# Optimization experiments

Hardware: AMD Instinct MI355X
Metric: run time of the kernel (lower is better)

The kernel has to match this reference:

```python
import jax, jax.numpy as jnp
import numpy as np

NB_CLASSES = 10  # matches init_kwargs nb_classes


def setup_inputs() -> dict:
    key = jax.random.key(0)
    k1, k2 = jax.random.split(key)
    N, D = 500_000, 64
    h = jax.random.normal(k1, (N, D), dtype=jnp.float32)
    yhat = jax.random.randint(k2, (N,), 0, NB_CLASSES, dtype=jnp.int32)
    return {"h": h, "yhat": yhat}


def reference(h, yhat):
    # Original torch loop: for each class k, gather h_k = h[yhat==k],
    # M_k = mean_i(h_i h_i^T) * 0.5 + I, loss += 0.5 * logdet(M_k).
    # mean of outer products == (masked h)^T @ h / count_k, so we avoid
    # the ragged gather and any [N, D, D] intermediate entirely.
    N, D = h.shape
    eye = jnp.eye(D, dtype=h.dtype)

    def class_term(k):
        mask = (yhat == k).astype(h.dtype)            # [N]
        count = jnp.sum(mask)                         # B_k
        gram = jnp.einsum('nd,ne->de', mask[:, None] * h, h)  # sum_i h_i h_i^T
        M = gram * (0.5 / count) + eye                # [D, D], SPD
        _, logabsdet = jnp.linalg.slogdet(M)
        return 0.5 * logabsdet

    # NB_CLASSES is a small fixed constant -> Python loop is fine & keeps
    # peak memory at one extra [N, D] buffer.
    return jnp.sum(jnp.stack([class_term(k) for k in range(NB_CLASSES)]))
```

## Files before the change

### kernel.cpp

```cpp
#include <hip/hip_runtime.h>
#include <hip/hip_bf16.h>

typedef __attribute__((ext_vector_type(8))) short    short8;
typedef __attribute__((ext_vector_type(4))) float    f32x4;
typedef __attribute__((ext_vector_type(4))) _Float16 f16x4;
typedef __attribute__((ext_vector_type(2))) unsigned u32x2;

#define NCLS 10
#define TILE 64
#define TPB  512
#define NQ   10
#define PPB  (NCLS * NQ * 256)
#define CH   16

#define AS1 __attribute__((address_space(1)))
#define AS3 __attribute__((address_space(3)))

#define MF(a, b, c) __builtin_amdgcn_mfma_f32_16x16x32_bf16((a), (b), (c), 0, 0, 0)

static __device__ __forceinline__ unsigned pkh2(float a, float b) {
    unsigned short ha = __builtin_bit_cast(unsigned short, (_Float16)a);
    unsigned short hb = __builtin_bit_cast(unsigned short, (_Float16)b);
    return (unsigned)ha | ((unsigned)hb << 16);
}

static __device__ __forceinline__ void issue_tile(
        const float* __restrict__ h, const int* __restrict__ yhat,
        float* fsb, int* yb, long t, long N, int wid, int lane) {
#pragma unroll
    for (int i = 0; i < 2; ++i) {
        const int C = (wid * 2 + i) * 64 + lane;
        long row = t * TILE + (C >> 4);
        if (row > N - 1) row = N - 1;
        const float* gp = h + row * 64 + ((C & 15) << 2);
        __builtin_amdgcn_global_load_lds((const AS1 float*)gp,
                                         (AS3 float*)(fsb + (wid * 2 + i) * 256),
                                         16, 0, 0);
    }
    if (wid == 0 && lane < 16) {
        long y0 = t * TILE + lane * 4;
        if (y0 > N - 4) y0 = N - 4;
        __builtin_amdgcn_global_load_lds((const AS1 int*)(yhat + y0),
                                         (AS3 int*)yb, 16, 0, 0);
    }
}

static __device__ __forceinline__ void compute_tile(
        const char* hsb, const char* mkb, int cls, int xcls, int wq,
        int hi, int col, f32x4 (&acc)[NQ], f32x4 (&accx)[3]) {
    const int sw = (col & 7) << 4;
#pragma unroll
    for (int ks = 0; ks < 2; ++ks) {
        const int b2 = ks * 64 + hi * 16;
        const short8 m = *(const short8*)(mkb + cls * 128 + b2);
        short8 raw[4], am[4];
#pragma unroll
        for (int nb = 0; nb < 4; ++nb) {
            raw[nb] = *(const short8*)(hsb + (nb * 16 + col) * 128 + (b2 ^ sw));
            am[nb]  = raw[nb] & m;
        }
        acc[0] = MF(am[0], am[0], acc[0]);
        acc[1] = MF(am[0], am[1], acc[1]);
        acc[2] = MF(am[0], am[2], acc[2]);
        acc[3] = MF(am[0], am[3], acc[3]);
        acc[4] = MF(am[1], am[1], acc[4]);
        acc[5] = MF(am[1], am[2], acc[5]);
        acc[6] = MF(am[1], am[3], acc[6]);
        acc[7] = MF(am[2], am[2], acc[7]);
        acc[8] = MF(am[2], am[3], acc[8]);
        acc[9] = MF(am[3], am[3], acc[9]);

        const short8 mx = *(const short8*)(mkb + xcls * 128 + b2);
        switch (wq) {
        case 0: { short8 x0 = raw[0] & mx, x1 = raw[1] & mx;
                  accx[0] = MF(x0, x0, accx[0]);
                  accx[1] = MF(x0, x1, accx[1]);
                  accx[2] = MF(x1, x1, accx[2]); } break;
        case 1: { short8 x0 = raw[0] & mx, x2 = raw[2] & mx, x3 = raw[3] & mx;
                  accx[0] = MF(x0, x2, accx[0]);
                  accx[1] = MF(x0, x3, accx[1]); } break;
        case 2: { short8 x1 = raw[1] & mx, x2 = raw[2] & mx, x3 = raw[3] & mx;
                  accx[0] = MF(x1, x2, accx[0]);
                  accx[1] = MF(x1, x3, accx[1]);
                  accx[2] = MF(x2, x2, accx[2]); } break;
        default:{ short8 x2 = raw[2] & mx, x3 = raw[3] & mx;
                  accx[0] = MF(x2, x3, accx[0]);
                  accx[1] = MF(x3, x3, accx[1]); } break;
        }
    }
}

__global__ __launch_bounds__(TPB, 4) void HL_gram(
        const float* __restrict__ h, const int* __restrict__ yhat,
        _Float16* __restrict__ partials, int* __restrict__ cntp,
        long N, int ntiles, int G) {
    __shared__ __align__(16) float          fs[3][TILE * 64];
    __shared__ __align__(16) unsigned short hs[2][64 * TILE];
    __shared__ __align__(16) unsigned short mk[2][NCLS * TILE];
    __shared__ __align__(16) int            ylds[3][TILE];

    const int tid  = threadIdx.x;
    const int wid  = tid >> 6;
    const int lane = tid & 63;
    const int hi   = lane >> 4;
    const int col  = lane & 15;

    const int cls  = wid;
    const int xcls = 8 + (wid >> 2);
    const int wq   = wid & 3;

    f32x4 acc[NQ], accx[3];
#pragma unroll
    for (int q = 0; q < NQ; ++q) acc[q] = (f32x4){0.f, 0.f, 0.f, 0.f};
#pragma unroll
    for (int q = 0; q < 3; ++q)  accx[q] = (f32x4){0.f, 0.f, 0.f, 0.f};
    int c0=0,c1=0,c2=0,c3=0,c4=0,c5=0,c6=0,c7=0,c8=0,c9=0;

    const int bid = blockIdx.x;
    const int K   = (ntiles - bid + G - 1) / G;

    issue_tile(h, yhat, &fs[0][0], &ylds[0][0], bid, N, wid, lane);
    if (K > 1)
        issue_tile(h, yhat, &fs[1][0], &ylds[1][0], bid + (long)G, N, wid, lane);

    for (int k = 0; k < K; ++k) {
        const long t  = bid + (long)k * G;
        const int  fk = k % 3;
        const int  hk = k & 1;

        if (k + 1 < K) {
            if (wid == 0) asm volatile("s_waitcnt vmcnt(3)" ::: "memory");
            else          asm volatile("s_waitcnt vmcnt(2)" ::: "memory");
        } else {
            asm volatile("s_waitcnt vmcnt(0)" ::: "memory");
        }
        asm volatile("s_waitcnt lgkmcnt(0)" ::: "memory");
        __builtin_amdgcn_s_barrier();
        __builtin_amdgcn_sched_barrier(0);

        {
            const float* fp = &fs[fk][0] + (wid * 8) * 64 + lane;
            float x[8];
#pragma unroll
            for (int j = 0; j < 8; ++j) x[j] = fp[j * 64];
            u32x2 lohi[2];
#pragma unroll
            for (int p = 0; p < 4; ++p) {
                __hip_bfloat162 pr = __float22bfloat162_rn(make_float2(x[2*p], x[2*p+1]));
                unsigned u;
                __builtin_memcpy(&u, &pr, 4);
                ((unsigned*)lohi)[p] = u;
            }
            char* hb = (char*)&hs[hk][0] + lane * 128 + ((wid * 16) ^ ((lane & 7) << 4));
            *(u32x2*)hb       = lohi[0];
            *(u32x2*)(hb + 8) = lohi[1];
        }
        if (wid == 7) {
            int y = ylds[fk][lane];
            if (t * TILE + lane >= N) y = -1;
            unsigned short* mb = &mk[hk][0];
#pragma unroll
            for (int c = 0; c < NCLS; ++c)
                mb[c * TILE + lane] = (y == c) ? (unsigned short)0xFFFFu
                                               : (unsigned short)0u;
            c0 += (int)__popcll(__ballot(y == 0));
            c1 += (int)__popcll(__ballot(y == 1));
            c2 += (int)__popcll(__ballot(y == 2));
            c3 += (int)__popcll(__ballot(y == 3));
            c4 += (int)__popcll(__ballot(y == 4));
            c5 += (int)__popcll(__ballot(y == 5));
            c6 += (int)__popcll(__ballot(y == 6));
            c7 += (int)__popcll(__ballot(y == 7));
            c8 += (int)__popcll(__ballot(y == 8));
            c9 += (int)__popcll(__ballot(y == 9));
        }

        if (k + 2 < K)
            issue_tile(h, yhat, &fs[(k + 2) % 3][0], &ylds[(k + 2) % 3][0],
                       bid + (long)(k + 2) * G, N, wid, lane);

        if (k > 0)
            compute_tile((const char*)&hs[hk ^ 1][0], (const char*)&mk[hk ^ 1][0],
                         cls, xcls, wq, hi, col, acc, accx);
    }

    asm volatile("s_waitcnt lgkmcnt(0)" ::: "memory");
    __builtin_amdgcn_s_barrier();
    __builtin_amdgcn_sched_barrier(0);
    compute_tile((const char*)&hs[(K - 1) & 1][0], (const char*)&mk[(K - 1) & 1][0],
                 cls, xcls, wq, hi, col, acc, accx);

    _Float16* pb = partials + (size_t)bid * PPB;
    {
        _Float16* po = pb + (size_t)cls * (NQ * 256);
#pragma unroll
        for (int q = 0; q < NQ; ++q) {
            u32x2 pk; pk[0] = pkh2(acc[q][0], acc[q][1]);
            pk[1] = pkh2(acc[q][2], acc[q][3]);
            *(u32x2*)(po + q * 256 + (lane << 2)) = pk;
        }
    }
    {
        _Float16* px = pb + (size_t)xcls * (NQ * 256) + (lane << 2);
        u32x2 pk0, pk1, pk2;
        pk0[0] = pkh2(accx[0][0], accx[0][1]); pk0[1] = pkh2(accx[0][2], accx[0][3]);
        pk1[0] = pkh2(accx[1][0], accx[1][1]); pk1[1] = pkh2(accx[1][2], accx[1][3]);
        pk2[0] = pkh2(accx[2][0], accx[2][1]); pk2[1] = pkh2(accx[2][2], accx[2][3]);
        switch (wq) {
        case 0: *(u32x2*)(px + 0 * 256) = pk0;
                *(u32x2*)(px + 1 * 256) = pk1;
                *(u32x2*)(px + 4 * 256) = pk2; break;
        case 1: *(u32x2*)(px + 2 * 256) = pk0;
                *(u32x2*)(px + 3 * 256) = pk1; break;
        case 2: *(u32x2*)(px + 5 * 256) = pk0;
                *(u32x2*)(px + 6 * 256) = pk1;
                *(u32x2*)(px + 7 * 256) = pk2; break;
        default:*(u32x2*)(px + 8 * 256) = pk0;
                *(u32x2*)(px + 9 * 256) = pk1; break;
        }
    }
    if (wid == 7 && lane == 0) {
        int* cp = cntp + bid * 16;
        cp[0]=c0; cp[1]=c1; cp[2]=c2; cp[3]=c3; cp[4]=c4;
        cp[5]=c5; cp[6]=c6; cp[7]=c7; cp[8]=c8; cp[9]=c9;
    }
}

__global__ void HL_reduce(const _Float16* __restrict__ partials, float* __restrict__ rpart,
                          float* __restrict__ out, int G, int CS) {
    const int idx = blockIdx.x * blockDim.x + threadIdx.x;
    if (blockIdx.x == 0 && threadIdx.x == 0) out[0] = 0.f;
    if (idx >= CH * NCLS * NQ * 64) return;
    const int ch = idx / (NCLS * NQ * 64);
    const int r  = idx % (NCLS * NQ * 64);
    const int cq = r >> 6;
    const int l  = r & 63;

    int b0 = ch * CS;
    int b1 = b0 + CS; if (b1 > G) b1 = G;

    f32x4 s = (f32x4){0.f, 0.f, 0.f, 0.f};
    const _Float16* p = partials + (size_t)cq * 256 + (l << 2);
    for (int b = b0; b < b1; ++b) {
        f16x4 v = *(const f16x4*)(p + (size_t)b * PPB);
        s[0] += (float)v[0]; s[1] += (float)v[1];
        s[2] += (float)v[2]; s[3] += (float)v[3];
    }
    *reinterpret_cast<f32x4*>(rpart + ((size_t)ch * (NCLS * NQ) + cq) * 256 + (l << 2)) = s;
}

__global__ __launch_bounds__(64, 1) void HL_chol(
        const float* __restrict__ rpart, const int* __restrict__ cntp,
        float* __restrict__ out, int G) {
    __shared__ float M[64][68];
    __shared__ float lcol[64];
    const int cls = blockIdx.x;
    const int i   = threadIdx.x;

    int c = 0;
    for (int b = i; b < G; b += 64) c += cntp[b * 16 + cls];
#pragma unroll
    for (int off = 32; off > 0; off >>= 1) c += __shfl_xor(c, off);
    const float inv = 0.5f / (float)c;

    const int QMB[NQ] = {0,0,0,0,1,1,1,2,2,3};
    const int QNB[NQ] = {0,1,2,3,1,2,3,2,3,3};
    const float* rp = rpart + (size_t)cls * (NQ * 256);
#pragma unroll
    for (int q = 0; q < NQ; ++q) {
        f32x4 s = (f32x4){0.f, 0.f, 0.f, 0.f};
#pragma unroll
        for (int ch = 0; ch < CH; ++ch)
            s += *reinterpret_cast<const f32x4*>(rp + (size_t)ch * (NCLS * NQ * 256) + q * 256 + (i << 2));
        const int row0 = QMB[q] * 16 + ((i >> 4) << 2);
        const int colo = QNB[q] * 16 + (i & 15);
#pragma unroll
        for (int rr = 0; rr < 4; ++rr) {
            M[row0 + rr][colo] = s[rr];
            M[colo][row0 + rr] = s[rr];
        }
    }
    __syncthreads();

    float row[64];
#pragma unroll
    for (int c2 = 0; c2 < 64; ++c2)
        row[c2] = M[i][c2] * inv + (c2 == i ? 1.0f : 0.0f);

#pragma unroll
    for (int j = 0; j < 64; ++j) {
        const float piv = __shfl(row[j], j);
        const float li  = row[j] * rsqrtf(piv);
        lcol[i] = li;
        __syncthreads();
#pragma unroll
        for (int c2 = j + 1; c2 < 64; ++c2)
            row[c2] -= li * lcol[c2];
        __syncthreads();
    }

    float slog = 0.f;
#pragma unroll
    for (int j = 0; j < 64; ++j)
        if (i == j) slog = __logf(row[j]);
    slog += __shfl_down(slog, 32); slog += __shfl_down(slog, 16);
    slog += __shfl_down(slog, 8);  slog += __shfl_down(slog, 4);
    slog += __shfl_down(slog, 2);  slog += __shfl_down(slog, 1);
    if (i == 0) atomicAdd(out, 0.5f * slog);
}

extern "C" void kernel_launch(void* const* d_in, const int* in_sizes, int n_in,
                              void* d_out, int out_size, void* d_ws, size_t ws_size,
                              hipStream_t stream) {
    const float* h    = (const float*)d_in[0];
    const int*   yhat = (const int*)d_in[1];
    const long   N    = in_sizes[1];
    float* out = (float*)d_out;

    const size_t rpart_sz = (size_t)CH * NCLS * NQ * 256 * sizeof(float);
    const size_t cntp_off = rpart_sz;

    const int ntiles = (int)((N + TILE - 1) / TILE);
    int G = 512;
    {
        const size_t perG = 64 + (size_t)PPB * sizeof(_Float16);
        if (ws_size > rpart_sz) {
            size_t maxG = (ws_size - rpart_sz) / perG;
            if ((size_t)G > maxG) G = (int)maxG;
        } else G = 1;
        if (G < 1) G = 1;
    }
    if (G > ntiles) G = ntiles;

    const size_t partials_off = cntp_off + (size_t)G * 16 * sizeof(int);
    float*    rpart    = (float*)d_ws;
    int*      cntp     = (int*)((char*)d_ws + cntp_off);
    _Float16* partials = (_Float16*)((char*)d_ws + partials_off);

    HL_gram<<<G, TPB, 0, stream>>>(h, yhat, partials, cntp, N, ntiles, G);

    int CS = (G + CH - 1) / CH;
    const int rthreads = CH * NCLS * NQ * 64;
    HL_reduce<<<(rthreads + 255) / 256, 256, 0, stream>>>(partials, rpart, out, G, CS);

    HL_chol<<<NCLS, 64, 0, stream>>>(rpart, cntp, out, G);
}
```

Before: 84.94 us.

## Restructure gram pipeline to double-buffer loads and stagger convert/compute across waves

Cuts the fp32 staging buffers from triple to double buffering with a single prefetch tile in flight and a full vmcnt(0) wait each iteration. Global addressing moves to 32-bit incrementing byte offsets with clamping, which removes 64-bit index math. Odd waves convert and then compute while even waves compute and then convert, so MFMA work and the bf16 conversion overlap across waves. The LDS read addressing in compute_tile is precomputed under a revised swizzle. The shallower prefetch risks exposing more memory latency, and the int offsets limit the input size.

```diff
diff --git a/kernel.cpp b/kernel.cpp
--- a/kernel.cpp
+++ b/kernel.cpp
@@ -24,39 +24,24 @@
     return (unsigned)ha | ((unsigned)hb << 16);
 }
 
-static __device__ __forceinline__ void issue_tile(
-        const float* __restrict__ h, const int* __restrict__ yhat,
-        float* fsb, int* yb, long t, long N, int wid, int lane) {
-#pragma unroll
-    for (int i = 0; i < 2; ++i) {
-        const int C = (wid * 2 + i) * 64 + lane;
-        long row = t * TILE + (C >> 4);
-        if (row > N - 1) row = N - 1;
-        const float* gp = h + row * 64 + ((C & 15) << 2);
-        __builtin_amdgcn_global_load_lds((const AS1 float*)gp,
-                                         (AS3 float*)(fsb + (wid * 2 + i) * 256),
-                                         16, 0, 0);
-    }
-    if (wid == 0 && lane < 16) {
-        long y0 = t * TILE + lane * 4;
-        if (y0 > N - 4) y0 = N - 4;
-        __builtin_amdgcn_global_load_lds((const AS1 int*)(yhat + y0),
-                                         (AS3 int*)yb, 16, 0, 0);
-    }
-}
-
 static __device__ __forceinline__ void compute_tile(
         const char* hsb, const char* mkb, int cls, int xcls, int wq,
         int hi, int col, f32x4 (&acc)[NQ], f32x4 (&accx)[3]) {
-    const int sw = (col & 7) << 4;
+    const int s56 = (col & 3) << 4;
+    const int s6  = (col & 4) << 4;
+    const char* rb0 = hsb + col * 128 + ((hi * 16) ^ s56) + s6;
+    const char* rb1 = hsb + col * 128 + ((hi * 16) ^ s56) + (64 ^ s6);
+    const char* mb  = mkb + cls  * 128 + hi * 16;
+    const char* xb  = mkb + xcls * 128 + hi * 16;
+
 #pragma unroll
     for (int ks = 0; ks < 2; ++ks) {
-        const int b2 = ks * 64 + hi * 16;
-        const short8 m = *(const short8*)(mkb + cls * 128 + b2);
+        const char* rb = ks ? rb1 : rb0;
+        const short8 m = *(const short8*)(mb + ks * 64);
         short8 raw[4], am[4];
 #pragma unroll
         for (int nb = 0; nb < 4; ++nb) {
-            raw[nb] = *(const short8*)(hsb + (nb * 16 + col) * 128 + (b2 ^ sw));
+            raw[nb] = *(const short8*)(rb + nb * 2048);
             am[nb]  = raw[nb] & m;
         }
         acc[0] = MF(am[0], am[0], acc[0]);
@@ -70,7 +55,7 @@
         acc[8] = MF(am[2], am[3], acc[8]);
         acc[9] = MF(am[3], am[3], acc[9]);
 
-        const short8 mx = *(const short8*)(mkb + xcls * 128 + b2);
+        const short8 mx = *(const short8*)(xb + ks * 64);
         switch (wq) {
         case 0: { short8 x0 = raw[0] & mx, x1 = raw[1] & mx;
                   accx[0] = MF(x0, x0, accx[0]);
@@ -93,11 +78,11 @@
 __global__ __launch_bounds__(TPB, 4) void HL_gram(
         const float* __restrict__ h, const int* __restrict__ yhat,
         _Float16* __restrict__ partials, int* __restrict__ cntp,
-        long N, int ntiles, int G) {
-    __shared__ __align__(16) float          fs[3][TILE * 64];
+        int N, int ntiles, int G) {
+    __shared__ __align__(16) float          fs[2][TILE * 64];
     __shared__ __align__(16) unsigned short hs[2][64 * TILE];
     __shared__ __align__(16) unsigned short mk[2][NCLS * TILE];
-    __shared__ __align__(16) int            ylds[3][TILE];
+    __shared__ __align__(16) int            ylds[2][TILE];
 
     const int tid  = threadIdx.x;
     const int wid  = tid >> 6;
@@ -119,69 +104,131 @@
     const int bid = blockIdx.x;
     const int K   = (ntiles - bid + G - 1) / G;
 
-    issue_tile(h, yhat, &fs[0][0], &ylds[0][0], bid, N, wid, lane);
-    if (K > 1)
-        issue_tile(h, yhat, &fs[1][0], &ylds[1][0], bid + (long)G, N, wid, lane);
+    const unsigned step   = (unsigned)G * TILE * 256u;
+    const unsigned maxoff = (unsigned)(N - 1) * 256u + (unsigned)(tid & 15) * 16u;
+    unsigned off0 = ((unsigned)bid * TILE + (unsigned)(tid >> 4)) * 256u
+                    + (unsigned)(tid & 15) * 16u;
+    const unsigned ystep  = (unsigned)G * TILE * 4u;
+    const unsigned maxy   = (unsigned)(N - 4) * 4u;
+    unsigned offy = (unsigned)bid * 256u + (unsigned)lane * 16u;
+    int rowN = bid * TILE + lane;
+
+    char* fdst0 = (char*)&fs[0][0] + wid * 1024;
+    char* fdst1 = (char*)&fs[1][0] + wid * 1024;
+
+    {
+        unsigned o0 = off0 > maxoff ? maxoff : off0;
+        unsigned o1 = off0 + 8192u; o1 = o1 > maxoff ? maxoff : o1;
+        __builtin_amdgcn_global_load_lds((const AS1 float*)((const char*)h + o0),
+                                         (AS3 float*)fdst0, 16, 0, 0);
+        __builtin_amdgcn_global_load_lds((const AS1 float*)((const char*)h + o1),
+                                         (AS3 float*)(fdst0 + 8192), 16, 0, 0);
+        if (wid == 7 && lane < 16) {
+            unsigned oy = offy > maxy ? maxy : offy;
+            __builtin_amdgcn_global_load_lds((const AS1 int*)((const char*)yhat + oy),
+                                             (AS3 int*)&ylds[0][0], 16, 0, 0);
+        }
+        off0 += step; offy += ystep;
+    }
 
     for (int k = 0; k < K; ++k) {
-        const long t  = bid + (long)k * G;
-        const int  fk = k % 3;
-        const int  hk = k & 1;
-
-        if (k + 1 < K) {
-            if (wid == 0) asm volatile("s_waitcnt vmcnt(3)" ::: "memory");
-            else          asm volatile("s_waitcnt vmcnt(2)" ::: "memory");
-        } else {
-            asm volatile("s_waitcnt vmcnt(0)" ::: "memory");
-        }
+        const int slot = k & 1;
+
+        asm volatile("s_waitcnt vmcnt(0)" ::: "memory");
         asm volatile("s_waitcnt lgkmcnt(0)" ::: "memory");
         __builtin_amdgcn_s_barrier();
         __builtin_amdgcn_sched_barrier(0);
 
-        {
-            const float* fp = &fs[fk][0] + (wid * 8) * 64 + lane;
-            float x[8];
-#pragma unroll
-            for (int j = 0; j < 8; ++j) x[j] = fp[j * 64];
-            u32x2 lohi[2];
-#pragma unroll
-            for (int p = 0; p < 4; ++p) {
-                __hip_bfloat162 pr = __float22bfloat162_rn(make_float2(x[2*p], x[2*p+1]));
-                unsigned u;
-                __builtin_memcpy(&u, &pr, 4);
-                ((unsigned*)lohi)[p] = u;
+        if (k + 1 < K) {
+            char* fd = slot ? fdst0 : fdst1;
+            unsigned o0 = off0 > maxoff ? maxoff : off0;
+            unsigned o1 = off0 + 8192u; o1 = o1 > maxoff ? maxoff : o1;
+            __builtin_amdgcn_global_load_lds((const AS1 float*)((const char*)h + o0),
+                                             (AS3 float*)fd, 16, 0, 0);
+            __builtin_amdgcn_global_load_lds((const AS1 float*)((const char*)h + o1),
+                                             (AS3 float*)(fd + 8192), 16, 0, 0);
+            if (wid == 7 && lane < 16) {
+                unsigned oy = offy > maxy ? maxy : offy;
+                __builtin_amdgcn_global_load_lds((const AS1 int*)((const char*)yhat + oy),
+                                                 (AS3 int*)&ylds[slot ^ 1][0], 16, 0, 0);
             }
-            char* hb = (char*)&hs[hk][0] + lane * 128 + ((wid * 16) ^ ((lane & 7) << 4));
-            *(u32x2*)hb       = lohi[0];
-            *(u32x2*)(hb + 8) = lohi[1];
-        }
-        if (wid == 7) {
-            int y = ylds[fk][lane];
-            if (t * TILE + lane >= N) y = -1;
-            unsigned short* mb = &mk[hk][0];
-#pragma unroll
-            for (int c = 0; c < NCLS; ++c)
-                mb[c * TILE + lane] = (y == c) ? (unsigned short)0xFFFFu
-                                               : (unsigned short)0u;
-            c0 += (int)__popcll(__ballot(y == 0));
-            c1 += (int)__popcll(__ballot(y == 1));
-            c2 += (int)__popcll(__ballot(y == 2));
-            c3 += (int)__popcll(__ballot(y == 3));
-            c4 += (int)__popcll(__ballot(y == 4));
-            c5 += (int)__popcll(__ballot(y == 5));
-            c6 += (int)__popcll(__ballot(y == 6));
-            c7 += (int)__popcll(__ballot(y == 7));
-            c8 += (int)__popcll(__ballot(y == 8));
-            c9 += (int)__popcll(__ballot(y == 9));
-        }
-
-        if (k + 2 < K)
-            issue_tile(h, yhat, &fs[(k + 2) % 3][0], &ylds[(k + 2) % 3][0],
-                       bid + (long)(k + 2) * G, N, wid, lane);
-
-        if (k > 0)
-            compute_tile((const char*)&hs[hk ^ 1][0], (const char*)&mk[hk ^ 1][0],
-                         cls, xcls, wq, hi, col, acc, accx);
+            off0 += step; offy += ystep;
+        }
+
+        const float* fsb = &fs[slot][0];
+        const char*  hsw = (const char*)&hs[slot][0];
+        const char*  hsr = (const char*)&hs[slot ^ 1][0];
+        const char*  mkw = (const char*)&mk[slot][0];
+        const char*  mkr = (const char*)&mk[slot ^ 1][0];
+
+        if (wid & 1) {
+            {
+                const float* fp = fsb + (wid * 8) * 64 + lane;
+                float x[8];
+#pragma unroll
+                for (int j = 0; j < 8; ++j) x[j] = fp[j * 64];
+                u32x2 lo, hi2;
+                lo[0]  = pkh2(0,0);
+                unsigned w0, w1, w2, w3;
+                {
+                    __hip_bfloat162 p0 = __float22bfloat162_rn(make_float2(x[0], x[1]));
+                    __hip_bfloat162 p1 = __float22bfloat162_rn(make_float2(x[2], x[3]));
+                    __hip_bfloat162 p2 = __float22bfloat162_rn(make_float2(x[4], x[5]));
+                    __hip_bfloat162 p3 = __float22bfloat162_rn(make_float2(x[6], x[7]));
+                    __builtin_memcpy(&w0, &p0, 4); __builtin_memcpy(&w1, &p1, 4);
+                    __builtin_memcpy(&w2, &p2, 4); __builtin_memcpy(&w3, &p3, 4);
+                }
+                lo[0] = w0; lo[1] = w1; hi2[0] = w2; hi2[1] = w3;
+                char* hb = (char*)hsw + lane * 128 + ((wid * 16) ^ ((lane & 7) << 4));
+                *(u32x2*)hb       = lo;
+                *(u32x2*)(hb + 8) = hi2;
+            }
+            if (wid == 7) {
+                int y = ylds[slot][lane];
+                if (rowN >= N) y = -1;
+                unsigned short* mbw = (unsigned short*)mkw;
+#pragma unroll
+                for (int c = 0; c < NCLS; ++c)
+                    mbw[c * TILE + lane] = (y == c) ? (unsigned short)0xFFFFu
+                                                    : (unsigned short)0u;
+                c0 += (int)__popcll(__ballot(y == 0));
+                c1 += (int)__popcll(__ballot(y == 1));
+                c2 += (int)__popcll(__ballot(y == 2));
+                c3 += (int)__popcll(__ballot(y == 3));
+                c4 += (int)__popcll(__ballot(y == 4));
+                c5 += (int)__popcll(__ballot(y == 5));
+                c6 += (int)__popcll(__ballot(y == 6));
+                c7 += (int)__popcll(__ballot(y == 7));
+                c8 += (int)__popcll(__ballot(y == 8));
+                c9 += (int)__popcll(__ballot(y == 9));
+                rowN += G * TILE;
+            }
+            if (k > 0)
+                compute_tile(hsr, mkr, cls, xcls, wq, hi, col, acc, accx);
+        } else {
+            if (k > 0)
+                compute_tile(hsr, mkr, cls, xcls, wq, hi, col, acc, accx);
+            {
+                const float* fp = fsb + (wid * 8) * 64 + lane;
+                float x[8];
+#pragma unroll
+                for (int j = 0; j < 8; ++j) x[j] = fp[j * 64];
+                unsigned w0, w1, w2, w3;
+                {
+                    __hip_bfloat162 p0 = __float22bfloat162_rn(make_float2(x[0], x[1]));
+                    __hip_bfloat162 p1 = __float22bfloat162_rn(make_float2(x[2], x[3]));
+                    __hip_bfloat162 p2 = __float22bfloat162_rn(make_float2(x[4], x[5]));
+                    __hip_bfloat162 p3 = __float22bfloat162_rn(make_float2(x[6], x[7]));
+                    __builtin_memcpy(&w0, &p0, 4); __builtin_memcpy(&w1, &p1, 4);
+                    __builtin_memcpy(&w2, &p2, 4); __builtin_memcpy(&w3, &p3, 4);
+                }
+                u32x2 lo, hi2;
+                lo[0] = w0; lo[1] = w1; hi2[0] = w2; hi2[1] = w3;
+                char* hb = (char*)hsw + lane * 128 + ((wid * 16) ^ ((lane & 7) << 4));
+                *(u32x2*)hb       = lo;
+                *(u32x2*)(hb + 8) = hi2;
+            }
+        }
     }
 
     asm volatile("s_waitcnt lgkmcnt(0)" ::: "memory");
@@ -314,13 +361,13 @@
                               hipStream_t stream) {
     const float* h    = (const float*)d_in[0];
     const int*   yhat = (const int*)d_in[1];
-    const long   N    = in_sizes[1];
+    const int    N    = in_sizes[1];
     float* out = (float*)d_out;
 
     const size_t rpart_sz = (size_t)CH * NCLS * NQ * 256 * sizeof(float);
     const size_t cntp_off = rpart_sz;
 
-    const int ntiles = (int)((N + TILE - 1) / TILE);
+    const int ntiles = (N + TILE - 1) / TILE;
     int G = 512;
     {
         const size_t perG = 64 + (size_t)PPB * sizeof(_Float16);
```

After: 90.38 us, median of 2. 6.4% more time.

## Replace LDS async staging with register double-buffered loads and ten-wave blocks

Applied to the files above, without the earlier changes.

Drops the global_load_lds fp32 staging buffers and instead loads each tile of h into registers, software-pipelined across two register sets, converting to bf16 straight into swizzled LDS. Tiles grow to 128 rows, and blocks grow to 10 waves: 8 waves each handle one class's gram, and 2 waves load labels and build masks, replacing the split cross-class work. Per-wave counts are merged through LDS atomics. This removes the fp32 LDS round trip and the uneven extra-class MFMA work, at the cost of more registers per thread and a barrier per tile.

```diff
diff --git a/kernel.cpp b/kernel.cpp
--- a/kernel.cpp
+++ b/kernel.cpp
@@ -5,60 +5,46 @@
 typedef __attribute__((ext_vector_type(4))) float    f32x4;
 typedef __attribute__((ext_vector_type(4))) _Float16 f16x4;
 typedef __attribute__((ext_vector_type(2))) unsigned u32x2;
+typedef __attribute__((ext_vector_type(4))) unsigned u32x4;
 
 #define NCLS 10
-#define TILE 64
-#define TPB  512
+#define TILE 128
+#define NW   10
+#define TPB  (NW * 64)
 #define NQ   10
 #define PPB  (NCLS * NQ * 256)
 #define CH   16
 
-#define AS1 __attribute__((address_space(1)))
-#define AS3 __attribute__((address_space(3)))
-
 #define MF(a, b, c) __builtin_amdgcn_mfma_f32_16x16x32_bf16((a), (b), (c), 0, 0, 0)
 
+static __device__ __forceinline__ unsigned pkbf2(float a, float b) {
+    __hip_bfloat162 p = __float22bfloat162_rn(make_float2(a, b));
+    unsigned u; __builtin_memcpy(&u, &p, 4);
+    return u;
+}
 static __device__ __forceinline__ unsigned pkh2(float a, float b) {
     unsigned short ha = __builtin_bit_cast(unsigned short, (_Float16)a);
     unsigned short hb = __builtin_bit_cast(unsigned short, (_Float16)b);
     return (unsigned)ha | ((unsigned)hb << 16);
 }
-
-static __device__ __forceinline__ void issue_tile(
-        const float* __restrict__ h, const int* __restrict__ yhat,
-        float* fsb, int* yb, long t, long N, int wid, int lane) {
-#pragma unroll
-    for (int i = 0; i < 2; ++i) {
-        const int C = (wid * 2 + i) * 64 + lane;
-        long row = t * TILE + (C >> 4);
-        if (row > N - 1) row = N - 1;
-        const float* gp = h + row * 64 + ((C & 15) << 2);
-        __builtin_amdgcn_global_load_lds((const AS1 float*)gp,
-                                         (AS3 float*)(fsb + (wid * 2 + i) * 256),
-                                         16, 0, 0);
-    }
-    if (wid == 0 && lane < 16) {
-        long y0 = t * TILE + lane * 4;
-        if (y0 > N - 4) y0 = N - 4;
-        __builtin_amdgcn_global_load_lds((const AS1 int*)(yhat + y0),
-                                         (AS3 int*)yb, 16, 0, 0);
-    }
+static __device__ __forceinline__ unsigned umin2(unsigned a, unsigned b) {
+    return a < b ? a : b;
 }
 
 static __device__ __forceinline__ void compute_tile(
-        const char* hsb, const char* mkb, int cls, int xcls, int wq,
-        int hi, int col, f32x4 (&acc)[NQ], f32x4 (&accx)[3]) {
-    const int sw = (col & 7) << 4;
-#pragma unroll
-    for (int ks = 0; ks < 2; ++ks) {
-        const int b2 = ks * 64 + hi * 16;
-        const short8 m = *(const short8*)(mkb + cls * 128 + b2);
-        short8 raw[4], am[4];
-#pragma unroll
-        for (int nb = 0; nb < 4; ++nb) {
-            raw[nb] = *(const short8*)(hsb + (nb * 16 + col) * 128 + (b2 ^ sw));
-            am[nb]  = raw[nb] & m;
-        }
+        const char* hsb, const char* mkb, int cls, int hi, int col,
+        f32x4 (&acc)[NQ]) {
+    const int r0 = col * 256 + ((hi * 16) ^ ((col & 7) << 4));
+    const int r1 = r0 ^ 64;
+    const char* mb = mkb + cls * 256 + hi * 16;
+#pragma unroll
+    for (int ks = 0; ks < 4; ++ks) {
+        const int ro = ((ks & 1) ? r1 : r0) + (ks >> 1) * 128;
+        const short8 m = *(const short8*)(mb + ks * 64);
+        short8 am[4];
+#pragma unroll
+        for (int nb = 0; nb < 4; ++nb)
+            am[nb] = *(const short8*)(hsb + ro + nb * 4096) & m;
         acc[0] = MF(am[0], am[0], acc[0]);
         acc[1] = MF(am[0], am[1], acc[1]);
         acc[2] = MF(am[0], am[2], acc[2]);
@@ -69,161 +55,141 @@
         acc[7] = MF(am[2], am[2], acc[7]);
         acc[8] = MF(am[2], am[3], acc[8]);
         acc[9] = MF(am[3], am[3], acc[9]);
-
-        const short8 mx = *(const short8*)(mkb + xcls * 128 + b2);
-        switch (wq) {
-        case 0: { short8 x0 = raw[0] & mx, x1 = raw[1] & mx;
-                  accx[0] = MF(x0, x0, accx[0]);
-                  accx[1] = MF(x0, x1, accx[1]);
-                  accx[2] = MF(x1, x1, accx[2]); } break;
-        case 1: { short8 x0 = raw[0] & mx, x2 = raw[2] & mx, x3 = raw[3] & mx;
-                  accx[0] = MF(x0, x2, accx[0]);
-                  accx[1] = MF(x0, x3, accx[1]); } break;
-        case 2: { short8 x1 = raw[1] & mx, x2 = raw[2] & mx, x3 = raw[3] & mx;
-                  accx[0] = MF(x1, x2, accx[0]);
-                  accx[1] = MF(x1, x3, accx[1]);
-                  accx[2] = MF(x2, x2, accx[2]); } break;
-        default:{ short8 x2 = raw[2] & mx, x3 = raw[3] & mx;
-                  accx[0] = MF(x2, x3, accx[0]);
-                  accx[1] = MF(x3, x3, accx[1]); } break;
-        }
-    }
-}
-
-__global__ __launch_bounds__(TPB, 4) void HL_gram(
+    }
+}
+
+__global__ __launch_bounds__(TPB, 5) void HL_gram(
         const float* __restrict__ h, const int* __restrict__ yhat,
         _Float16* __restrict__ partials, int* __restrict__ cntp,
-        long N, int ntiles, int G) {
-    __shared__ __align__(16) float          fs[3][TILE * 64];
+        int N, int ntiles, int G) {
     __shared__ __align__(16) unsigned short hs[2][64 * TILE];
     __shared__ __align__(16) unsigned short mk[2][NCLS * TILE];
-    __shared__ __align__(16) int            ylds[3][TILE];
+    __shared__ int cntlds[16];
 
     const int tid  = threadIdx.x;
     const int wid  = tid >> 6;
     const int lane = tid & 63;
     const int hi   = lane >> 4;
     const int col  = lane & 15;
-
     const int cls  = wid;
-    const int xcls = 8 + (wid >> 2);
-    const int wq   = wid & 3;
-
-    f32x4 acc[NQ], accx[3];
+
+    if (tid < 16) cntlds[tid] = 0;
+
+    f32x4 acc[NQ];
 #pragma unroll
     for (int q = 0; q < NQ; ++q) acc[q] = (f32x4){0.f, 0.f, 0.f, 0.f};
-#pragma unroll
-    for (int q = 0; q < 3; ++q)  accx[q] = (f32x4){0.f, 0.f, 0.f, 0.f};
     int c0=0,c1=0,c2=0,c3=0,c4=0,c5=0,c6=0,c7=0,c8=0,c9=0;
 
     const int bid = blockIdx.x;
     const int K   = (ntiles - bid + G - 1) / G;
 
-    issue_tile(h, yhat, &fs[0][0], &ylds[0][0], bid, N, wid, lane);
-    if (K > 1)
-        issue_tile(h, yhat, &fs[1][0], &ylds[1][0], bid + (long)G, N, wid, lane);
-
-    for (int k = 0; k < K; ++k) {
-        const long t  = bid + (long)k * G;
-        const int  fk = k % 3;
-        const int  hk = k & 1;
-
-        if (k + 1 < K) {
-            if (wid == 0) asm volatile("s_waitcnt vmcnt(3)" ::: "memory");
-            else          asm volatile("s_waitcnt vmcnt(2)" ::: "memory");
-        } else {
-            asm volatile("s_waitcnt vmcnt(0)" ::: "memory");
-        }
-        asm volatile("s_waitcnt lgkmcnt(0)" ::: "memory");
-        __builtin_amdgcn_s_barrier();
+    const unsigned maxh = (unsigned)(N - 8) * 256u + (unsigned)lane * 4u;
+    const unsigned maxy = (unsigned)(N - 1) * 4u;
+    const int yhalf = (wid - 8) * 64;
+
+    float xA[16], xB[16];
+    int   yA = -1, yB = -1;
+
+#define STAGE(X, t)                                                            \
+    {                                                                          \
+        if (wid < 8) {                                                         \
+            const unsigned ub = (unsigned)(t) * (TILE * 256u)                  \
+                              + (unsigned)wid * 2048u + (unsigned)lane * 4u;   \
+            const unsigned o0 = umin2(ub, maxh);                               \
+            const unsigned o1 = umin2(ub + 16384u, maxh);                      \
+            _Pragma("unroll")                                                  \
+            for (int j = 0; j < 8; ++j)                                        \
+                x##X[j] = *(const float*)((const char*)h + o0 + j * 256);      \
+            _Pragma("unroll")                                                  \
+            for (int j = 0; j < 8; ++j)                                        \
+                x##X[8 + j] = *(const float*)((const char*)h + o1 + j * 256);  \
+        } else {                                                               \
+            const unsigned oy = umin2((unsigned)(t) * (TILE * 4u)              \
+                                      + (unsigned)(lane + yhalf) * 4u, maxy);  \
+            y##X = *(const int*)((const char*)yhat + oy);                      \
+        }                                                                      \
+    }
+
+#define CONVERT(X, slot, t)                                                    \
+    {                                                                          \
+        if (wid < 8) {                                                         \
+            u32x4 vlo, vhi;                                                    \
+            vlo[0] = pkbf2(x##X[0],  x##X[1]);                                 \
+            vlo[1] = pkbf2(x##X[2],  x##X[3]);                                 \
+            vlo[2] = pkbf2(x##X[4],  x##X[5]);                                 \
+            vlo[3] = pkbf2(x##X[6],  x##X[7]);                                 \
+            vhi[0] = pkbf2(x##X[8],  x##X[9]);                                 \
+            vhi[1] = pkbf2(x##X[10], x##X[11]);                                \
+            vhi[2] = pkbf2(x##X[12], x##X[13]);                                \
+            vhi[3] = pkbf2(x##X[14], x##X[15]);                                \
+            char* hb = (char*)&hs[slot][0] + lane * 256                        \
+                       + ((wid * 16) ^ ((lane & 7) << 4));                     \
+            *(u32x4*)hb         = vlo;                                         \
+            *(u32x4*)(hb + 128) = vhi;                                         \
+        } else {                                                               \
+            int y = y##X;                                                      \
+            if ((t) * TILE + lane + yhalf >= N) y = -1;                        \
+            unsigned short* mw = &mk[slot][0];                                 \
+            const int r = lane + yhalf;                                        \
+            _Pragma("unroll")                                                  \
+            for (int c = 0; c < NCLS; ++c)                                     \
+                mw[c * TILE + r] = (y == c) ? (unsigned short)0xFFFFu          \
+                                            : (unsigned short)0u;              \
+            c0 += (int)__popcll(__ballot(y == 0));                             \
+            c1 += (int)__popcll(__ballot(y == 1));                             \
+            c2 += (int)__popcll(__ballot(y == 2));                             \
+            c3 += (int)__popcll(__ballot(y == 3));                             \
+            c4 += (int)__popcll(__ballot(y == 4));                             \
+            c5 += (int)__popcll(__ballot(y == 5));                             \
+            c6 += (int)__popcll(__ballot(y == 6));                             \
+            c7 += (int)__popcll(__ballot(y == 7));                             \
+            c8 += (int)__popcll(__ballot(y == 8));                             \
+            c9 += (int)__popcll(__ballot(y == 9));                             \
+        }                                                                      \
+    }
+
+#define BAR()                                                                  \
+    asm volatile("s_waitcnt lgkmcnt(0)" ::: "memory");                         \
+    __builtin_amdgcn_s_barrier();                                              \
+    __builtin_amdgcn_sched_barrier(0);
+
+    STAGE(A, bid);
+
+    for (int k = 0; k < K; k += 2) {
+        if (k + 1 < K) STAGE(B, bid + (k + 1) * G);
         __builtin_amdgcn_sched_barrier(0);
-
-        {
-            const float* fp = &fs[fk][0] + (wid * 8) * 64 + lane;
-            float x[8];
-#pragma unroll
-            for (int j = 0; j < 8; ++j) x[j] = fp[j * 64];
-            u32x2 lohi[2];
-#pragma unroll
-            for (int p = 0; p < 4; ++p) {
-                __hip_bfloat162 pr = __float22bfloat162_rn(make_float2(x[2*p], x[2*p+1]));
-                unsigned u;
-                __builtin_memcpy(&u, &pr, 4);
-                ((unsigned*)lohi)[p] = u;
-            }
-            char* hb = (char*)&hs[hk][0] + lane * 128 + ((wid * 16) ^ ((lane & 7) << 4));
-            *(u32x2*)hb       = lohi[0];
-            *(u32x2*)(hb + 8) = lohi[1];
-        }
-        if (wid == 7) {
-            int y = ylds[fk][lane];
-            if (t * TILE + lane >= N) y = -1;
-            unsigned short* mb = &mk[hk][0];
-#pragma unroll
-            for (int c = 0; c < NCLS; ++c)
-                mb[c * TILE + lane] = (y == c) ? (unsigned short)0xFFFFu
-                                               : (unsigned short)0u;
-            c0 += (int)__popcll(__ballot(y == 0));
-            c1 += (int)__popcll(__ballot(y == 1));
-            c2 += (int)__popcll(__ballot(y == 2));
-            c3 += (int)__popcll(__ballot(y == 3));
-            c4 += (int)__popcll(__ballot(y == 4));
-            c5 += (int)__popcll(__ballot(y == 5));
-            c6 += (int)__popcll(__ballot(y == 6));
-            c7 += (int)__popcll(__ballot(y == 7));
-            c8 += (int)__popcll(__ballot(y == 8));
-            c9 += (int)__popcll(__ballot(y == 9));
-        }
-
-        if (k + 2 < K)
-            issue_tile(h, yhat, &fs[(k + 2) % 3][0], &ylds[(k + 2) % 3][0],
-                       bid + (long)(k + 2) * G, N, wid, lane);
-
-        if (k > 0)
-            compute_tile((const char*)&hs[hk ^ 1][0], (const char*)&mk[hk ^ 1][0],
-                         cls, xcls, wq, hi, col, acc, accx);
-    }
-
-    asm volatile("s_waitcnt lgkmcnt(0)" ::: "memory");
-    __builtin_amdgcn_s_barrier();
-    __builtin_amdgcn_sched_barrier(0);
-    compute_tile((const char*)&hs[(K - 1) & 1][0], (const char*)&mk[(K - 1) & 1][0],
-                 cls, xcls, wq, hi, col, acc, accx);
-
-    _Float16* pb = partials + (size_t)bid * PPB;
-    {
-        _Float16* po = pb + (size_t)cls * (NQ * 256);
-#pragma unroll
-        for (int q = 0; q < NQ; ++q) {
-            u32x2 pk; pk[0] = pkh2(acc[q][0], acc[q][1]);
-            pk[1] = pkh2(acc[q][2], acc[q][3]);
-            *(u32x2*)(po + q * 256 + (lane << 2)) = pk;
-        }
-    }
-    {
-        _Float16* px = pb + (size_t)xcls * (NQ * 256) + (lane << 2);
-        u32x2 pk0, pk1, pk2;
-        pk0[0] = pkh2(accx[0][0], accx[0][1]); pk0[1] = pkh2(accx[0][2], accx[0][3]);
-        pk1[0] = pkh2(accx[1][0], accx[1][1]); pk1[1] = pkh2(accx[1][2], accx[1][3]);
-        pk2[0] = pkh2(accx[2][0], accx[2][1]); pk2[1] = pkh2(accx[2][2], accx[2][3]);
-        switch (wq) {
-        case 0: *(u32x2*)(px + 0 * 256) = pk0;
-                *(u32x2*)(px + 1 * 256) = pk1;
-                *(u32x2*)(px + 4 * 256) = pk2; break;
-        case 1: *(u32x2*)(px + 2 * 256) = pk0;
-                *(u32x2*)(px + 3 * 256) = pk1; break;
-        case 2: *(u32x2*)(px + 5 * 256) = pk0;
-                *(u32x2*)(px + 6 * 256) = pk1;
-                *(u32x2*)(px + 7 * 256) = pk2; break;
-        default:*(u32x2*)(px + 8 * 256) = pk0;
-                *(u32x2*)(px + 9 * 256) = pk1; break;
-        }
-    }
-    if (wid == 7 && lane == 0) {
-        int* cp = cntp + bid * 16;
-        cp[0]=c0; cp[1]=c1; cp[2]=c2; cp[3]=c3; cp[4]=c4;
-        cp[5]=c5; cp[6]=c6; cp[7]=c7; cp[8]=c8; cp[9]=c9;
-    }
+        CONVERT(A, 0, bid + k * G);
+        BAR();
+        compute_tile((const char*)&hs[0][0], (const char*)&mk[0][0],
+                     cls, hi, col, acc);
+        if (k + 1 >= K) break;
+
+        if (k + 2 < K) STAGE(A, bid + (k + 2) * G);
+        __builtin_amdgcn_sched_barrier(0);
+        CONVERT(B, 1, bid + (k + 1) * G);
+        BAR();
+        compute_tile((const char*)&hs[1][0], (const char*)&mk[1][0],
+                     cls, hi, col, acc);
+    }
+
+    if (wid >= 8 && lane == 0) {
+        atomicAdd(&cntlds[0], c0); atomicAdd(&cntlds[1], c1);
+        atomicAdd(&cntlds[2], c2); atomicAdd(&cntlds[3], c3);
+        atomicAdd(&cntlds[4], c4); atomicAdd(&cntlds[5], c5);
+        atomicAdd(&cntlds[6], c6); atomicAdd(&cntlds[7], c7);
+        atomicAdd(&cntlds[8], c8); atomicAdd(&cntlds[9], c9);
+    }
+    __syncthreads();
+
+    _Float16* po = partials + (size_t)bid * PPB + (size_t)cls * (NQ * 256);
+#pragma unroll
+    for (int q = 0; q < NQ; ++q) {
+        u32x2 pk;
+        pk[0] = pkh2(acc[q][0], acc[q][1]);
+        pk[1] = pkh2(acc[q][2], acc[q][3]);
+        *(u32x2*)(po + q * 256 + (lane << 2)) = pk;
+    }
+    if (tid < NCLS) cntp[bid * 16 + tid] = cntlds[tid];
 }
 
 __global__ void HL_reduce(const _Float16* __restrict__ partials, float* __restrict__ rpart,
@@ -314,13 +280,13 @@
                               hipStream_t stream) {
     const float* h    = (const float*)d_in[0];
     const int*   yhat = (const int*)d_in[1];
-    const long   N    = in_sizes[1];
+    const int    N    = in_sizes[1];
     float* out = (float*)d_out;
 
     const size_t rpart_sz = (size_t)CH * NCLS * NQ * 256 * sizeof(float);
     const size_t cntp_off = rpart_sz;
 
-    const int ntiles = (int)((N + TILE - 1) / TILE);
+    const int ntiles = (N + TILE - 1) / TILE;
     int G = 512;
     {
         const size_t perG = 64 + (size_t)PPB * sizeof(_Float16);
```

Result: slower. 286.0 us (+236.7%).
